# Kernel tuning notes

Measured on AMD Instinct MI355X. Metric: run time of the kernel, lower is better.

The kernel has to match this reference:

```python
import jax, jax.numpy as jnp
import numpy as np

B, NC, T = 256, 10, 4096
EPS, ALPHA, GAMMA, MU = 0.2, 0.5, 1e-4, 8e-4


def setup_inputs() -> dict:
    key = jax.random.key(0)
    k1, k2, k3 = jax.random.split(key, 3)
    scores = jax.random.uniform(k1, (B * NC, T), dtype=jnp.float32)
    attw = jax.random.uniform(k2, (B * NC, T), dtype=jnp.float32)
    # first half abnormal (label=1), second half normal (label=0), as pfu.unbag assumes
    label = jnp.concatenate([jnp.ones(B // 2, jnp.int32), jnp.zeros(B // 2, jnp.int32)])
    seqlen = jax.random.randint(k3, (B,), 128, T + 1, dtype=jnp.int32)
    return {"scores": scores, "attw": attw, "label": label, "seqlen": seqlen}


def _bce_neg(p, mask, slen):  # BCE vs all-zeros target, mean over valid length
    l = jnp.maximum(jnp.log(1.0 - p), -100.0)  # torch BCELoss clamps log at -100
    return -jnp.sum(jnp.where(mask, l, 0.0), axis=1) / slen


def _bce_pos(p, mask, slen):  # BCE vs all-ones target
    l = jnp.maximum(jnp.log(p), -100.0)
    return -jnp.sum(jnp.where(mask, l, 0.0), axis=1) / slen


def reference(scores, attw, label, seqlen):
    Bn = label.shape[0]
    nc = scores.shape[0] // Bn
    Tn = scores.shape[1]
    # pfu.uncrop(x, 'mean'): average over crops -> [B, T]
    sc = scores.reshape(Bn, nc, Tn).mean(axis=1)
    aw = attw.reshape(Bn, nc, Tn).mean(axis=1)
    bdiv = Bn // 2
    # pfu.unbag: abnormal = first half (label==1), normal = second half
    S1, A1, sl1i = sc[:bdiv], aw[:bdiv], seqlen[:bdiv]
    S0, A0, sl0i = sc[bdiv:], aw[bdiv:], seqlen[bdiv:]
    sl1 = sl1i.astype(jnp.float32)
    sl0 = sl0i.astype(jnp.float32)
    t = jnp.arange(Tn)[None, :]
    m1 = t < sl1i[:, None]  # valid-position masks (ragged slicing)
    m0 = t < sl0i[:, None]
    SA0 = A0 * S0
    SA1 = A1 * S1

    def theta(A, m):  # (max - min) * eps + min over valid region
        mx = jnp.max(jnp.where(m, A, -jnp.inf), axis=1)
        mn = jnp.min(jnp.where(m, A, jnp.inf), axis=1)
        return (mx - mn) * EPS + mn

    sup0 = (A0 < theta(A0, m0)[:, None]) & m0
    sup1 = (A1 < theta(A1, m1)[:, None]) & m1
    SSO0 = S0 * sup0
    SSA0 = SA0 * sup0
    SSO1 = S1 * sup1
    SSA1 = SA1 * sup1

    LC_SO = _bce_neg(S0, m0, sl0) + _bce_pos(S1, m1, sl1)
    LC_SA = _bce_neg(SA0, m0, sl0) + _bce_pos(SA1, m1, sl1)
    LC_SSO = _bce_neg(SSO0, m0, sl0) + _bce_pos(SSO1, m1, sl1)
    LC_SSA = _bce_neg(SSA0, m0, sl0) + _bce_pos(SSA1, m1, sl1)

    LN_1 = jnp.sum(jnp.where(m1, jnp.abs(A1), 0.0), axis=1)

    # LG_0 / LG_1 are overwritten in the torch loop -> only last batch item counts
    LG_0 = jnp.sum(jnp.where(m0[-1], A0[-1] ** 2, 0.0)) / sl0[-1]
    # cur_stp = 1 < M  ->  lg1_tmp = SO_1 (soft guide)
    LG_1 = jnp.sum(jnp.where(m1[-1], (A1[-1] - S1[-1]) ** 2, 0.0)) / sl1[-1]

    dm0 = t[:, : Tn - 1] < (sl0i - 1)[:, None]  # valid adjacent-diff positions
    dm1 = t[:, : Tn - 1] < (sl1i - 1)[:, None]

    def smt(S, dm):
        return jnp.sum(jnp.where(dm, (S[:, :-1] - S[:, 1:]) ** 2, 0.0), axis=1)

    LSmt = smt(S0, dm0) + smt(S1, dm1) + smt(SA0, dm0) + smt(SA1, dm1)
    LSpr = (jnp.sum(jnp.where(m0, S0, 0.0), axis=1) + jnp.sum(jnp.where(m1, S1, 0.0), axis=1)
            + jnp.sum(jnp.where(m0, SA0, 0.0), axis=1) + jnp.sum(jnp.where(m1, SA1, 0.0), axis=1))

    return jnp.stack([
        (ALPHA * LC_SO).mean(),          # slclas_og
        (ALPHA * LC_SA).mean(),          # slclas_att
        ((1.0 - ALPHA) * LC_SSO).mean(), # slclas_supog
        ((1.0 - ALPHA) * LC_SSA).mean(), # slclas_supatt
        (GAMMA * LN_1).mean(),           # norm_1
        LG_0,                            # guide_0
        LG_1,                            # guide_1
        (MU * LSmt).mean(),              # smooth
        LSpr.mean(),                     # sparse
    ])
```

## Files before the change

kernel.cpp:

```cpp
#include <hip/hip_runtime.h>
#include <math.h>

constexpr int   T_DIM = 4096;
constexpr int   NC    = 10;
constexpr int   NTHR  = 1024;
constexpr int   NWAVE = NTHR / 64;
constexpr int   PSTRIDE = 16;

constexpr float EPS_C   = 0.2f;
constexpr float ALPHA_C = 0.5f;
constexpr float GAMMA_C = 1e-4f;
constexpr float MU_C    = 8e-4f;

__global__ __launch_bounds__(NTHR) void mbs_pass1(
    const float* __restrict__ scores,
    const float* __restrict__ attw,
    const int*   __restrict__ seqlen,
    float*       __restrict__ part,
    int B)
{
    __shared__ float s_lds[T_DIM];
    __shared__ float a_lds[T_DIM];
    __shared__ float red_mx[NWAVE];
    __shared__ float red_mn[NWAVE];
    __shared__ float red_sum[NWAVE][8];
    __shared__ float sh_theta;

    const int tid  = threadIdx.x;
    const int lane = tid & 63;
    const int wid  = tid >> 6;
    const int b    = blockIdx.x;
    const int slen = seqlen[b];
    const bool pos = b < (B >> 1);
    const int t0   = tid * 4;
    const bool active = t0 < slen;

    float4 s4 = make_float4(0.f, 0.f, 0.f, 0.f);
    float4 a4 = make_float4(0.f, 0.f, 0.f, 0.f);
    if (active) {
        const size_t rowbase = (size_t)b * NC * T_DIM + t0;
#pragma unroll
        for (int c = 0; c < NC; ++c) {
            const float4 sv = *reinterpret_cast<const float4*>(scores + rowbase + (size_t)c * T_DIM);
            const float4 av = *reinterpret_cast<const float4*>(attw   + rowbase + (size_t)c * T_DIM);
            s4.x += sv.x; s4.y += sv.y; s4.z += sv.z; s4.w += sv.w;
            a4.x += av.x; a4.y += av.y; a4.z += av.z; a4.w += av.w;
        }
        const float invNC = 1.0f / (float)NC;
        s4.x *= invNC; s4.y *= invNC; s4.z *= invNC; s4.w *= invNC;
        a4.x *= invNC; a4.y *= invNC; a4.z *= invNC; a4.w *= invNC;

        reinterpret_cast<float4*>(s_lds)[tid] = s4;
        reinterpret_cast<float4*>(a_lds)[tid] = a4;
    }

    const float sarr[4] = {s4.x, s4.y, s4.z, s4.w};
    const float aarr[4] = {a4.x, a4.y, a4.z, a4.w};

    float amax = -INFINITY, amin = INFINITY;
    if (active) {
#pragma unroll
        for (int j = 0; j < 4; ++j) {
            if (t0 + j < slen) {
                amax = fmaxf(amax, aarr[j]);
                amin = fminf(amin, aarr[j]);
            }
        }
    }
#pragma unroll
    for (int off = 32; off; off >>= 1) {
        amax = fmaxf(amax, __shfl_down(amax, off, 64));
        amin = fminf(amin, __shfl_down(amin, off, 64));
    }
    if (lane == 0) { red_mx[wid] = amax; red_mn[wid] = amin; }
    __syncthreads();
    if (tid == 0) {
        float mx = red_mx[0], mn = red_mn[0];
#pragma unroll
        for (int w = 1; w < NWAVE; ++w) {
            mx = fmaxf(mx, red_mx[w]);
            mn = fminf(mn, red_mn[w]);
        }
        sh_theta = (mx - mn) * EPS_C + mn;
    }
    __syncthreads();
    const float theta = sh_theta;

    float v0 = 0.f, v1 = 0.f, v2 = 0.f, v3 = 0.f,
          v4 = 0.f, v5 = 0.f, v6 = 0.f, v7 = 0.f;
    const bool isLG = (b == (B >> 1) - 1) || (b == B - 1);

    if (active) {
#pragma unroll
        for (int j = 0; j < 4; ++j) {
            const int t   = t0 + j;
            const float s  = sarr[j];
            const float a  = aarr[j];
            const float sa = s * a;
            if (t < slen) {
                const bool sup = a < theta;
                if (pos) {
                    const float ls  = fmaxf(__logf(s),  -100.0f);
                    const float lsa = fmaxf(__logf(sa), -100.0f);
                    v0 += ls;
                    v1 += lsa;
                    v2 += sup ? ls  : -100.0f;
                    v3 += sup ? lsa : -100.0f;
                    v4 += fabsf(a);
                    if (isLG) v5 += (a - s) * (a - s);
                } else {
                    const float ls  = fmaxf(__logf(1.0f - s),  -100.0f);
                    const float lsa = fmaxf(__logf(1.0f - sa), -100.0f);
                    v0 += ls;
                    v1 += lsa;
                    if (sup) { v2 += ls; v3 += lsa; }
                    if (isLG) v5 += a * a;
                }
                v7 += s + sa;
            }
            if (t < slen - 1) {
                const float s2 = (j < 3) ? sarr[j + 1] : s_lds[t + 1];
                const float a2 = (j < 3) ? aarr[j + 1] : a_lds[t + 1];
                const float ds  = s  - s2;
                const float dsa = sa - s2 * a2;
                v6 += ds * ds + dsa * dsa;
            }
        }
    }

    float vals[8] = {v0, v1, v2, v3, v4, v5, v6, v7};
#pragma unroll
    for (int k = 0; k < 8; ++k) {
#pragma unroll
        for (int off = 32; off; off >>= 1)
            vals[k] += __shfl_down(vals[k], off, 64);
    }
    if (lane == 0) {
#pragma unroll
        for (int k = 0; k < 8; ++k) red_sum[wid][k] = vals[k];
    }
    __syncthreads();

    if (tid == 0) {
        float tot[8];
#pragma unroll
        for (int k = 0; k < 8; ++k) tot[k] = 0.f;
        for (int w = 0; w < NWAVE; ++w)
#pragma unroll
            for (int k = 0; k < 8; ++k) tot[k] += red_sum[w][k];

        const float inv_slen = 1.0f / (float)slen;
        const float invB2    = 2.0f / (float)B;

        float* p = part + (size_t)b * PSTRIDE;
        p[0] = ALPHA_C          * (-tot[0] * inv_slen) * invB2;
        p[1] = ALPHA_C          * (-tot[1] * inv_slen) * invB2;
        p[2] = (1.0f - ALPHA_C) * (-tot[2] * inv_slen) * invB2;
        p[3] = (1.0f - ALPHA_C) * (-tot[3] * inv_slen) * invB2;
        p[4] = pos ? (GAMMA_C * tot[4] * invB2) : 0.0f;
        p[5] = (b == B - 1)        ? tot[5] * inv_slen : 0.0f;
        p[6] = (b == (B >> 1) - 1) ? tot[5] * inv_slen : 0.0f;
        p[7] = MU_C * tot[6] * invB2;
        p[8] = tot[7] * invB2;
    }
}

__global__ __launch_bounds__(64) void mbs_pass2(
    const float* __restrict__ part,
    float*       __restrict__ out,
    int B)
{
    float acc[9];
#pragma unroll
    for (int k = 0; k < 9; ++k) acc[k] = 0.f;
    for (int r = (int)threadIdx.x; r < B; r += 64) {
        const float* p = part + (size_t)r * PSTRIDE;
#pragma unroll
        for (int k = 0; k < 9; ++k) acc[k] += p[k];
    }
#pragma unroll
    for (int k = 0; k < 9; ++k) {
#pragma unroll
        for (int off = 32; off; off >>= 1)
            acc[k] += __shfl_down(acc[k], off, 64);
    }
    if (threadIdx.x == 0) {
#pragma unroll
        for (int k = 0; k < 9; ++k) out[k] = acc[k];
    }
}

extern "C" void kernel_launch(void* const* d_in, const int* in_sizes, int n_in,
                              void* d_out, int out_size, void* d_ws, size_t ws_size,
                              hipStream_t stream) {
    const float* scores = (const float*)d_in[0];
    const float* attw   = (const float*)d_in[1];
    const int*   seqlen = (const int*)d_in[3];
    const int B = in_sizes[2];

    float* part = (float*)d_ws;

    mbs_pass1<<<dim3(B), dim3(NTHR), 0, stream>>>(scores, attw, seqlen, part, B);
    mbs_pass2<<<dim3(1), dim3(64), 0, stream>>>(part, (float*)d_out, B);
}
```

Measured before the change: 19.55 us.

## Split each row across four chunk blocks with global staging and last-block reduction

Each row now runs as four 256-thread blocks instead of one 1024-thread block, which raises the number of blocks in flight. The first kernel writes the crop means to global workspace along with per-chunk max/min and partial sums. The second kernel computes theta from the chunk extrema, rereads the means to get the suppressed and smoothness terms, and has the last block (chosen by an atomic counter) do the final reduction. This drops the separate reduction launch, but it adds a global round trip for the means and puts the log work in two passes.

Measured after the change: 40.32 us. +106.2%, slower.

```diff
diff --git a/kernel.cpp b/kernel.cpp
--- a/kernel.cpp
+++ b/kernel.cpp
@@ -3,124 +3,200 @@
 
 constexpr int   T_DIM = 4096;
 constexpr int   NC    = 10;
-constexpr int   NTHR  = 1024;
+constexpr int   CHUNK = 1024;
+constexpr int   NCH   = T_DIM / CHUNK;
+constexpr int   NTHR  = CHUNK / 4;
 constexpr int   NWAVE = NTHR / 64;
-constexpr int   PSTRIDE = 16;
 
 constexpr float EPS_C   = 0.2f;
 constexpr float ALPHA_C = 0.5f;
 constexpr float GAMMA_C = 1e-4f;
 constexpr float MU_C    = 8e-4f;
 
-__global__ __launch_bounds__(NTHR) void mbs_pass1(
+
+__global__ __launch_bounds__(NTHR) void mbs_k1(
     const float* __restrict__ scores,
     const float* __restrict__ attw,
     const int*   __restrict__ seqlen,
-    float*       __restrict__ part,
+    float*       __restrict__ ws,
     int B)
 {
-    __shared__ float s_lds[T_DIM];
-    __shared__ float a_lds[T_DIM];
-    __shared__ float red_mx[NWAVE];
-    __shared__ float red_mn[NWAVE];
-    __shared__ float red_sum[NWAVE][8];
-    __shared__ float sh_theta;
-
+    float* Smean = ws;
+    float* Amean = ws + (size_t)B * T_DIM;
+    float* cmax  = Amean + (size_t)B * T_DIM;
+    float* cmin  = cmax + (size_t)B * NCH;
+    float* P1    = cmin + (size_t)B * NCH;
+    unsigned int* cnt =
+        (unsigned int*)(P1 + (size_t)B * NCH * 8 + (size_t)B * NCH * 4);
+
+    const int bid  = blockIdx.x;
+    const int row  = bid / NCH;
+    const int ch   = bid - row * NCH;
     const int tid  = threadIdx.x;
     const int lane = tid & 63;
     const int wid  = tid >> 6;
-    const int b    = blockIdx.x;
-    const int slen = seqlen[b];
-    const bool pos = b < (B >> 1);
-    const int t0   = tid * 4;
+
+    if (bid == 0 && tid == 0) *cnt = 0u;
+
+    const int  slen   = seqlen[row];
+    const bool pos    = row < (B >> 1);
+    const bool isLG   = (row == (B >> 1) - 1) || (row == B - 1);
+    const int  t0     = ch * CHUNK + tid * 4;
     const bool active = t0 < slen;
 
     float4 s4 = make_float4(0.f, 0.f, 0.f, 0.f);
     float4 a4 = make_float4(0.f, 0.f, 0.f, 0.f);
     if (active) {
-        const size_t rowbase = (size_t)b * NC * T_DIM + t0;
+        const size_t base = (size_t)row * NC * T_DIM + t0;
 #pragma unroll
         for (int c = 0; c < NC; ++c) {
-            const float4 sv = *reinterpret_cast<const float4*>(scores + rowbase + (size_t)c * T_DIM);
-            const float4 av = *reinterpret_cast<const float4*>(attw   + rowbase + (size_t)c * T_DIM);
+            const float4 sv = *reinterpret_cast<const float4*>(scores + base + (size_t)c * T_DIM);
+            const float4 av = *reinterpret_cast<const float4*>(attw   + base + (size_t)c * T_DIM);
             s4.x += sv.x; s4.y += sv.y; s4.z += sv.z; s4.w += sv.w;
             a4.x += av.x; a4.y += av.y; a4.z += av.z; a4.w += av.w;
         }
         const float invNC = 1.0f / (float)NC;
         s4.x *= invNC; s4.y *= invNC; s4.z *= invNC; s4.w *= invNC;
         a4.x *= invNC; a4.y *= invNC; a4.z *= invNC; a4.w *= invNC;
-
-        reinterpret_cast<float4*>(s_lds)[tid] = s4;
-        reinterpret_cast<float4*>(a_lds)[tid] = a4;
+        *reinterpret_cast<float4*>(Smean + (size_t)row * T_DIM + t0) = s4;
+        *reinterpret_cast<float4*>(Amean + (size_t)row * T_DIM + t0) = a4;
     }
 
     const float sarr[4] = {s4.x, s4.y, s4.z, s4.w};
     const float aarr[4] = {a4.x, a4.y, a4.z, a4.w};
 
-    float amax = -INFINITY, amin = INFINITY;
+    float mx = -INFINITY, mn = INFINITY;
+    float v0 = 0.f, v1 = 0.f, v4 = 0.f, v5 = 0.f, v7 = 0.f;
     if (active) {
 #pragma unroll
         for (int j = 0; j < 4; ++j) {
-            if (t0 + j < slen) {
-                amax = fmaxf(amax, aarr[j]);
-                amin = fminf(amin, aarr[j]);
-            }
-        }
-    }
+            const int t = t0 + j;
+            if (t < slen) {
+                const float s  = sarr[j];
+                const float a  = aarr[j];
+                const float sa = s * a;
+                mx = fmaxf(mx, a);
+                mn = fminf(mn, a);
+                if (pos) {
+                    v0 += fmaxf(__logf(s),  -100.0f);
+                    v1 += fmaxf(__logf(sa), -100.0f);
+                    v4 += fabsf(a);
+                    if (isLG) v5 += (a - s) * (a - s);
+                } else {
+                    v0 += fmaxf(__logf(1.0f - s),  -100.0f);
+                    v1 += fmaxf(__logf(1.0f - sa), -100.0f);
+                    if (isLG) v5 += a * a;
+                }
+                v7 += s + sa;
+            }
+        }
+    }
+
+    float vals[7] = {mx, mn, v0, v1, v4, v5, v7};
 #pragma unroll
     for (int off = 32; off; off >>= 1) {
-        amax = fmaxf(amax, __shfl_down(amax, off, 64));
-        amin = fminf(amin, __shfl_down(amin, off, 64));
-    }
-    if (lane == 0) { red_mx[wid] = amax; red_mn[wid] = amin; }
+        vals[0] = fmaxf(vals[0], __shfl_down(vals[0], off, 64));
+        vals[1] = fminf(vals[1], __shfl_down(vals[1], off, 64));
+#pragma unroll
+        for (int k = 2; k < 7; ++k)
+            vals[k] += __shfl_down(vals[k], off, 64);
+    }
+    __shared__ float red[NWAVE][7];
+    if (lane == 0)
+#pragma unroll
+        for (int k = 0; k < 7; ++k) red[wid][k] = vals[k];
     __syncthreads();
+
     if (tid == 0) {
-        float mx = red_mx[0], mn = red_mn[0];
+        float tmx = red[0][0], tmn = red[0][1];
+        float t2 = red[0][2], t3 = red[0][3], t4 = red[0][4],
+              t5 = red[0][5], t6 = red[0][6];
 #pragma unroll
         for (int w = 1; w < NWAVE; ++w) {
-            mx = fmaxf(mx, red_mx[w]);
-            mn = fminf(mn, red_mn[w]);
-        }
-        sh_theta = (mx - mn) * EPS_C + mn;
-    }
-    __syncthreads();
-    const float theta = sh_theta;
-
-    float v0 = 0.f, v1 = 0.f, v2 = 0.f, v3 = 0.f,
-          v4 = 0.f, v5 = 0.f, v6 = 0.f, v7 = 0.f;
-    const bool isLG = (b == (B >> 1) - 1) || (b == B - 1);
-
+            tmx = fmaxf(tmx, red[w][0]);
+            tmn = fminf(tmn, red[w][1]);
+            t2 += red[w][2]; t3 += red[w][3]; t4 += red[w][4];
+            t5 += red[w][5]; t6 += red[w][6];
+        }
+        cmax[(size_t)row * NCH + ch] = tmx;
+        cmin[(size_t)row * NCH + ch] = tmn;
+
+        const float inv_slen = 1.0f / (float)slen;
+        const float invB2    = 2.0f / (float)B;
+        float* p = P1 + (size_t)bid * 8;
+        p[0] = ALPHA_C * (-t2 * inv_slen) * invB2;
+        p[1] = ALPHA_C * (-t3 * inv_slen) * invB2;
+        p[2] = pos ? (GAMMA_C * t4 * invB2) : 0.0f;
+        p[3] = (row == B - 1)        ? t5 * inv_slen : 0.0f;
+        p[4] = (row == (B >> 1) - 1) ? t5 * inv_slen : 0.0f;
+        p[5] = t6 * invB2;
+    }
+}
+
+__global__ __launch_bounds__(NTHR) void mbs_k2(
+    const int* __restrict__ seqlen,
+    float*     __restrict__ ws,
+    float*     __restrict__ out,
+    int B)
+{
+    float* Smean = ws;
+    float* Amean = ws + (size_t)B * T_DIM;
+    float* cmax  = Amean + (size_t)B * T_DIM;
+    float* cmin  = cmax + (size_t)B * NCH;
+    float* P1    = cmin + (size_t)B * NCH;
+    float* P2    = P1 + (size_t)B * NCH * 8;
+    unsigned int* cnt = (unsigned int*)(P2 + (size_t)B * NCH * 4);
+
+    const int bid  = blockIdx.x;
+    const int grid = gridDim.x;
+    const int row  = bid / NCH;
+    const int ch   = bid - row * NCH;
+    const int tid  = threadIdx.x;
+    const int lane = tid & 63;
+    const int wid  = tid >> 6;
+
+    const int  slen   = seqlen[row];
+    const bool pos    = row < (B >> 1);
+    const int  t0     = ch * CHUNK + tid * 4;
+    const bool active = t0 < slen;
+
+    float mx = -INFINITY, mn = INFINITY;
+#pragma unroll
+    for (int c = 0; c < NCH; ++c) {
+        mx = fmaxf(mx, cmax[(size_t)row * NCH + c]);
+        mn = fminf(mn, cmin[(size_t)row * NCH + c]);
+    }
+    const float theta = (mx - mn) * EPS_C + mn;
+
+    float v2 = 0.f, v3 = 0.f, v6 = 0.f;
     if (active) {
+        const float4 s4 = *reinterpret_cast<const float4*>(Smean + (size_t)row * T_DIM + t0);
+        const float4 a4 = *reinterpret_cast<const float4*>(Amean + (size_t)row * T_DIM + t0);
+        const float sarr[4] = {s4.x, s4.y, s4.z, s4.w};
+        const float aarr[4] = {a4.x, a4.y, a4.z, a4.w};
 #pragma unroll
         for (int j = 0; j < 4; ++j) {
-            const int t   = t0 + j;
+            const int t = t0 + j;
             const float s  = sarr[j];
             const float a  = aarr[j];
             const float sa = s * a;
             if (t < slen) {
                 const bool sup = a < theta;
                 if (pos) {
-                    const float ls  = fmaxf(__logf(s),  -100.0f);
-                    const float lsa = fmaxf(__logf(sa), -100.0f);
-                    v0 += ls;
-                    v1 += lsa;
-                    v2 += sup ? ls  : -100.0f;
-                    v3 += sup ? lsa : -100.0f;
-                    v4 += fabsf(a);
-                    if (isLG) v5 += (a - s) * (a - s);
-                } else {
-                    const float ls  = fmaxf(__logf(1.0f - s),  -100.0f);
-                    const float lsa = fmaxf(__logf(1.0f - sa), -100.0f);
-                    v0 += ls;
-                    v1 += lsa;
-                    if (sup) { v2 += ls; v3 += lsa; }
-                    if (isLG) v5 += a * a;
+                    v2 += sup ? fmaxf(__logf(s),  -100.0f) : -100.0f;
+                    v3 += sup ? fmaxf(__logf(sa), -100.0f) : -100.0f;
+                } else if (sup) {
+                    v2 += fmaxf(__logf(1.0f - s),  -100.0f);
+                    v3 += fmaxf(__logf(1.0f - sa), -100.0f);
                 }
-                v7 += s + sa;
             }
             if (t < slen - 1) {
-                const float s2 = (j < 3) ? sarr[j + 1] : s_lds[t + 1];
-                const float a2 = (j < 3) ? aarr[j + 1] : a_lds[t + 1];
+                float s2, a2;
+                if (j < 3) { s2 = sarr[j + 1]; a2 = aarr[j + 1]; }
+                else {
+                    s2 = Smean[(size_t)row * T_DIM + t + 1];
+                    a2 = Amean[(size_t)row * T_DIM + t + 1];
+                }
                 const float ds  = s  - s2;
                 const float dsa = sa - s2 * a2;
                 v6 += ds * ds + dsa * dsa;
@@ -128,65 +204,71 @@
         }
     }
 
-    float vals[8] = {v0, v1, v2, v3, v4, v5, v6, v7};
-#pragma unroll
-    for (int k = 0; k < 8; ++k) {
-#pragma unroll
-        for (int off = 32; off; off >>= 1)
+    float vals[3] = {v2, v3, v6};
+#pragma unroll
+    for (int off = 32; off; off >>= 1)
+#pragma unroll
+        for (int k = 0; k < 3; ++k)
             vals[k] += __shfl_down(vals[k], off, 64);
-    }
-    if (lane == 0) {
-#pragma unroll
-        for (int k = 0; k < 8; ++k) red_sum[wid][k] = vals[k];
-    }
+
+    __shared__ float red[NWAVE][3];
+    __shared__ int   sdone;
+    if (lane == 0)
+#pragma unroll
+        for (int k = 0; k < 3; ++k) red[wid][k] = vals[k];
     __syncthreads();
 
     if (tid == 0) {
-        float tot[8];
-#pragma unroll
-        for (int k = 0; k < 8; ++k) tot[k] = 0.f;
-        for (int w = 0; w < NWAVE; ++w)
-#pragma unroll
-            for (int k = 0; k < 8; ++k) tot[k] += red_sum[w][k];
-
+        float t2 = red[0][0], t3 = red[0][1], t6 = red[0][2];
+#pragma unroll
+        for (int w = 1; w < NWAVE; ++w) {
+            t2 += red[w][0]; t3 += red[w][1]; t6 += red[w][2];
+        }
         const float inv_slen = 1.0f / (float)slen;
         const float invB2    = 2.0f / (float)B;
-
-        float* p = part + (size_t)b * PSTRIDE;
-        p[0] = ALPHA_C          * (-tot[0] * inv_slen) * invB2;
-        p[1] = ALPHA_C          * (-tot[1] * inv_slen) * invB2;
-        p[2] = (1.0f - ALPHA_C) * (-tot[2] * inv_slen) * invB2;
-        p[3] = (1.0f - ALPHA_C) * (-tot[3] * inv_slen) * invB2;
-        p[4] = pos ? (GAMMA_C * tot[4] * invB2) : 0.0f;
-        p[5] = (b == B - 1)        ? tot[5] * inv_slen : 0.0f;
-        p[6] = (b == (B >> 1) - 1) ? tot[5] * inv_slen : 0.0f;
-        p[7] = MU_C * tot[6] * invB2;
-        p[8] = tot[7] * invB2;
-    }
-}
-
-__global__ __launch_bounds__(64) void mbs_pass2(
-    const float* __restrict__ part,
-    float*       __restrict__ out,
-    int B)
-{
-    float acc[9];
-#pragma unroll
-    for (int k = 0; k < 9; ++k) acc[k] = 0.f;
-    for (int r = (int)threadIdx.x; r < B; r += 64) {
-        const float* p = part + (size_t)r * PSTRIDE;
-#pragma unroll
-        for (int k = 0; k < 9; ++k) acc[k] += p[k];
-    }
-#pragma unroll
-    for (int k = 0; k < 9; ++k) {
+        float* p = P2 + (size_t)bid * 4;
+        p[0] = (1.0f - ALPHA_C) * (-t2 * inv_slen) * invB2;
+        p[1] = (1.0f - ALPHA_C) * (-t3 * inv_slen) * invB2;
+        p[2] = MU_C * t6 * invB2;
+        __threadfence();
+        const unsigned int old = atomicAdd(cnt, 1u);
+        sdone = (old == (unsigned int)(grid - 1)) ? 1 : 0;
+    }
+    __syncthreads();
+
+    if (sdone) {
+        __threadfence();
+        float acc[9];
+#pragma unroll
+        for (int k = 0; k < 9; ++k) acc[k] = 0.f;
+        for (int i = tid; i < grid; i += NTHR) {
+            const float* p1 = P1 + (size_t)i * 8;
+            const float* p2 = P2 + (size_t)i * 4;
+            acc[0] += p1[0]; acc[1] += p1[1];
+            acc[2] += p2[0]; acc[3] += p2[1];
+            acc[4] += p1[2]; acc[5] += p1[3];
+            acc[6] += p1[4]; acc[7] += p2[2];
+            acc[8] += p1[5];
+        }
 #pragma unroll
         for (int off = 32; off; off >>= 1)
-            acc[k] += __shfl_down(acc[k], off, 64);
-    }
-    if (threadIdx.x == 0) {
-#pragma unroll
-        for (int k = 0; k < 9; ++k) out[k] = acc[k];
+#pragma unroll
+            for (int k = 0; k < 9; ++k)
+                acc[k] += __shfl_down(acc[k], off, 64);
+        __shared__ float redf[NWAVE][9];
+        if (lane == 0)
+#pragma unroll
+            for (int k = 0; k < 9; ++k) redf[wid][k] = acc[k];
+        __syncthreads();
+        if (tid == 0) {
+#pragma unroll
+            for (int k = 0; k < 9; ++k) {
+                float s = redf[0][k];
+#pragma unroll
+                for (int w = 1; w < NWAVE; ++w) s += redf[w][k];
+                out[k] = s;
+            }
+        }
     }
 }
 
@@ -197,9 +279,10 @@
     const float* attw   = (const float*)d_in[1];
     const int*   seqlen = (const int*)d_in[3];
     const int B = in_sizes[2];
-
-    float* part = (float*)d_ws;
-
-    mbs_pass1<<<dim3(B), dim3(NTHR), 0, stream>>>(scores, attw, seqlen, part, B);
-    mbs_pass2<<<dim3(1), dim3(64), 0, stream>>>(part, (float*)d_out, B);
+    const int grid = B * NCH;
+
+    mbs_k1<<<dim3(grid), dim3(NTHR), 0, stream>>>(scores, attw, seqlen,
+                                                  (float*)d_ws, B);
+    mbs_k2<<<dim3(grid), dim3(NTHR), 0, stream>>>(seqlen, (float*)d_ws,
+                                                  (float*)d_out, B);
 }
```

## Split crop-mean into windowed kernel with direct global-to-LDS loads

Applied to the files above, without the earlier changes.

The crop-averaging stage moves into a new kernel launched over B*8 blocks, each handling one 512-column window. Each block loads all crops into LDS with global_load_lds, writes the mean rows to workspace and records per-window attention max/min. A second kernel combines the window max/min into theta and computes the losses from the stored means. The goal is more parallelism and better memory-level parallelism for the bandwidth-heavy crop reads, paid for by an extra launch and a workspace round trip for the means.

Result: slower. 26.70 us (+36.5%).

```diff
diff --git a/kernel.cpp b/kernel.cpp
--- a/kernel.cpp
+++ b/kernel.cpp
@@ -3,8 +3,10 @@
 
 constexpr int   T_DIM = 4096;
 constexpr int   NC    = 10;
-constexpr int   NTHR  = 1024;
-constexpr int   NWAVE = NTHR / 64;
+constexpr int   WIN   = 512;
+constexpr int   NQ    = T_DIM / WIN;
+constexpr int   K2THR = 1024;
+constexpr int   K2WAVE = K2THR / 64;
 constexpr int   PSTRIDE = 16;
 
 constexpr float EPS_C   = 0.2f;
@@ -12,88 +14,153 @@
 constexpr float GAMMA_C = 1e-4f;
 constexpr float MU_C    = 8e-4f;
 
-__global__ __launch_bounds__(NTHR) void mbs_pass1(
+
+__device__ __forceinline__ void gl_lds16(const float* g, float* l) {
+    __builtin_amdgcn_global_load_lds(
+        (const __attribute__((address_space(1))) void*)g,
+        (__attribute__((address_space(3))) void*)l, 16, 0, 0);
+}
+
+__global__ __launch_bounds__(256) void mbs_k1(
     const float* __restrict__ scores,
     const float* __restrict__ attw,
     const int*   __restrict__ seqlen,
-    float*       __restrict__ part,
+    float*       __restrict__ ws,
     int B)
 {
+    float* Smean = ws;
+    float* Amean = ws + (size_t)B * T_DIM;
+    float* cmax  = Amean + (size_t)B * T_DIM;
+    float* cmin  = cmax + (size_t)B * NQ;
+
+    __shared__ float sl[NC][WIN];
+    __shared__ float al[NC][WIN];
+
+    const int bid  = blockIdx.x;
+    const int row  = bid >> 3;
+    const int win  = bid & 7;
+    const int tid  = threadIdx.x;
+    const int lane = tid & 63;
+    const int w    = tid >> 6;
+    const int slen = seqlen[row];
+    const int c0   = win * WIN;
+
+    if (c0 >= slen) {
+        if (tid == 0) {
+            cmax[row * NQ + win] = -INFINITY;
+            cmin[row * NQ + win] =  INFINITY;
+        }
+        return;
+    }
+
+    const size_t rowbase = (size_t)row * NC * T_DIM;
+    const bool   hi      = (c0 + 256) < slen;
+#pragma unroll
+    for (int i = 0; i < 10; ++i) {
+        const int piece = w * 10 + i;
+        const int half  = piece / 20;
+        const int rem   = piece % 20;
+        const int c     = rem >> 1;
+        const int part  = rem & 1;
+        if (part == 0 || hi) {
+            const float* g = (half ? attw : scores)
+                           + rowbase + (size_t)c * T_DIM + c0 + part * 256 + lane * 4;
+            float* l = (half ? &al[0][0] : &sl[0][0]) + c * WIN + part * 256;
+            gl_lds16(g, l);
+        }
+    }
+    __syncthreads();
+
+    const size_t rowm = (size_t)row * T_DIM;
+    const int  cc  = 2 * tid;
+    const int  col = c0 + cc;
+    const bool act = col < slen;
+    float amx = -INFINITY, amn = INFINITY;
+    if (act) {
+        float s0 = 0.f, s1 = 0.f, a0 = 0.f, a1 = 0.f;
+#pragma unroll
+        for (int c = 0; c < NC; ++c) {
+            const float2 sv = *reinterpret_cast<const float2*>(&sl[c][cc]);
+            const float2 av = *reinterpret_cast<const float2*>(&al[c][cc]);
+            s0 += sv.x; s1 += sv.y;
+            a0 += av.x; a1 += av.y;
+        }
+        const float2 sm = make_float2(s0 * 0.1f, s1 * 0.1f);
+        const float2 am = make_float2(a0 * 0.1f, a1 * 0.1f);
+        *reinterpret_cast<float2*>(Smean + rowm + col) = sm;
+        *reinterpret_cast<float2*>(Amean + rowm + col) = am;
+        amx = am.x; amn = am.x;
+        if (col + 1 < slen) { amx = fmaxf(amx, am.y); amn = fminf(amn, am.y); }
+    }
+
+#pragma unroll
+    for (int off = 32; off; off >>= 1) {
+        amx = fmaxf(amx, __shfl_down(amx, off, 64));
+        amn = fminf(amn, __shfl_down(amn, off, 64));
+    }
+    __syncthreads();
+    if (lane == 0) { sl[0][w] = amx; sl[0][4 + w] = amn; }
+    __syncthreads();
+    if (tid == 0) {
+        const float mx = fmaxf(fmaxf(sl[0][0], sl[0][1]), fmaxf(sl[0][2], sl[0][3]));
+        const float mn = fminf(fminf(sl[0][4], sl[0][5]), fminf(sl[0][6], sl[0][7]));
+        cmax[row * NQ + win] = mx;
+        cmin[row * NQ + win] = mn;
+    }
+}
+
+__global__ __launch_bounds__(K2THR) void mbs_k2(
+    const int*   __restrict__ seqlen,
+    const float* __restrict__ ws,
+    float*       __restrict__ part2,
+    int B)
+{
+    const float* Smean = ws;
+    const float* Amean = ws + (size_t)B * T_DIM;
+    const float* cmax  = Amean + (size_t)B * T_DIM;
+    const float* cmin  = cmax + (size_t)B * NQ;
+
     __shared__ float s_lds[T_DIM];
     __shared__ float a_lds[T_DIM];
-    __shared__ float red_mx[NWAVE];
-    __shared__ float red_mn[NWAVE];
-    __shared__ float red_sum[NWAVE][8];
-    __shared__ float sh_theta;
-
+    __shared__ float red_sum[K2WAVE][8];
+
+    const int b    = blockIdx.x;
     const int tid  = threadIdx.x;
     const int lane = tid & 63;
     const int wid  = tid >> 6;
-    const int b    = blockIdx.x;
     const int slen = seqlen[b];
     const bool pos = b < (B >> 1);
+    const bool isLG = (b == (B >> 1) - 1) || (b == B - 1);
     const int t0   = tid * 4;
     const bool active = t0 < slen;
+
+    float mx = -INFINITY, mn = INFINITY;
+#pragma unroll
+    for (int c = 0; c < NQ; ++c) {
+        mx = fmaxf(mx, cmax[b * NQ + c]);
+        mn = fminf(mn, cmin[b * NQ + c]);
+    }
+    const float theta = (mx - mn) * EPS_C + mn;
 
     float4 s4 = make_float4(0.f, 0.f, 0.f, 0.f);
     float4 a4 = make_float4(0.f, 0.f, 0.f, 0.f);
     if (active) {
-        const size_t rowbase = (size_t)b * NC * T_DIM + t0;
-#pragma unroll
-        for (int c = 0; c < NC; ++c) {
-            const float4 sv = *reinterpret_cast<const float4*>(scores + rowbase + (size_t)c * T_DIM);
-            const float4 av = *reinterpret_cast<const float4*>(attw   + rowbase + (size_t)c * T_DIM);
-            s4.x += sv.x; s4.y += sv.y; s4.z += sv.z; s4.w += sv.w;
-            a4.x += av.x; a4.y += av.y; a4.z += av.z; a4.w += av.w;
-        }
-        const float invNC = 1.0f / (float)NC;
-        s4.x *= invNC; s4.y *= invNC; s4.z *= invNC; s4.w *= invNC;
-        a4.x *= invNC; a4.y *= invNC; a4.z *= invNC; a4.w *= invNC;
-
+        s4 = *reinterpret_cast<const float4*>(Smean + (size_t)b * T_DIM + t0);
+        a4 = *reinterpret_cast<const float4*>(Amean + (size_t)b * T_DIM + t0);
         reinterpret_cast<float4*>(s_lds)[tid] = s4;
         reinterpret_cast<float4*>(a_lds)[tid] = a4;
     }
+    __syncthreads();
 
     const float sarr[4] = {s4.x, s4.y, s4.z, s4.w};
     const float aarr[4] = {a4.x, a4.y, a4.z, a4.w};
 
-    float amax = -INFINITY, amin = INFINITY;
-    if (active) {
-#pragma unroll
-        for (int j = 0; j < 4; ++j) {
-            if (t0 + j < slen) {
-                amax = fmaxf(amax, aarr[j]);
-                amin = fminf(amin, aarr[j]);
-            }
-        }
-    }
-#pragma unroll
-    for (int off = 32; off; off >>= 1) {
-        amax = fmaxf(amax, __shfl_down(amax, off, 64));
-        amin = fminf(amin, __shfl_down(amin, off, 64));
-    }
-    if (lane == 0) { red_mx[wid] = amax; red_mn[wid] = amin; }
-    __syncthreads();
-    if (tid == 0) {
-        float mx = red_mx[0], mn = red_mn[0];
-#pragma unroll
-        for (int w = 1; w < NWAVE; ++w) {
-            mx = fmaxf(mx, red_mx[w]);
-            mn = fminf(mn, red_mn[w]);
-        }
-        sh_theta = (mx - mn) * EPS_C + mn;
-    }
-    __syncthreads();
-    const float theta = sh_theta;
-
     float v0 = 0.f, v1 = 0.f, v2 = 0.f, v3 = 0.f,
           v4 = 0.f, v5 = 0.f, v6 = 0.f, v7 = 0.f;
-    const bool isLG = (b == (B >> 1) - 1) || (b == B - 1);
-
     if (active) {
 #pragma unroll
         for (int j = 0; j < 4; ++j) {
-            const int t   = t0 + j;
+            const int t = t0 + j;
             const float s  = sarr[j];
             const float a  = aarr[j];
             const float sa = s * a;
@@ -130,29 +197,26 @@
 
     float vals[8] = {v0, v1, v2, v3, v4, v5, v6, v7};
 #pragma unroll
-    for (int k = 0; k < 8; ++k) {
+    for (int k = 0; k < 8; ++k)
 #pragma unroll
         for (int off = 32; off; off >>= 1)
             vals[k] += __shfl_down(vals[k], off, 64);
-    }
-    if (lane == 0) {
+    if (lane == 0)
 #pragma unroll
         for (int k = 0; k < 8; ++k) red_sum[wid][k] = vals[k];
-    }
     __syncthreads();
 
     if (tid == 0) {
         float tot[8];
 #pragma unroll
         for (int k = 0; k < 8; ++k) tot[k] = 0.f;
-        for (int w = 0; w < NWAVE; ++w)
-#pragma unroll
-            for (int k = 0; k < 8; ++k) tot[k] += red_sum[w][k];
+        for (int w2 = 0; w2 < K2WAVE; ++w2)
+#pragma unroll
+            for (int k = 0; k < 8; ++k) tot[k] += red_sum[w2][k];
 
         const float inv_slen = 1.0f / (float)slen;
         const float invB2    = 2.0f / (float)B;
-
-        float* p = part + (size_t)b * PSTRIDE;
+        float* p = part2 + (size_t)b * PSTRIDE;
         p[0] = ALPHA_C          * (-tot[0] * inv_slen) * invB2;
         p[1] = ALPHA_C          * (-tot[1] * inv_slen) * invB2;
         p[2] = (1.0f - ALPHA_C) * (-tot[2] * inv_slen) * invB2;
@@ -165,8 +229,8 @@
     }
 }
 
-__global__ __launch_bounds__(64) void mbs_pass2(
-    const float* __restrict__ part,
+__global__ __launch_bounds__(64) void mbs_k3(
+    const float* __restrict__ part2,
     float*       __restrict__ out,
     int B)
 {
@@ -174,20 +238,18 @@
 #pragma unroll
     for (int k = 0; k < 9; ++k) acc[k] = 0.f;
     for (int r = (int)threadIdx.x; r < B; r += 64) {
-        const float* p = part + (size_t)r * PSTRIDE;
+        const float* p = part2 + (size_t)r * PSTRIDE;
 #pragma unroll
         for (int k = 0; k < 9; ++k) acc[k] += p[k];
     }
 #pragma unroll
-    for (int k = 0; k < 9; ++k) {
+    for (int k = 0; k < 9; ++k)
 #pragma unroll
         for (int off = 32; off; off >>= 1)
             acc[k] += __shfl_down(acc[k], off, 64);
-    }
-    if (threadIdx.x == 0) {
+    if (threadIdx.x == 0)
 #pragma unroll
         for (int k = 0; k < 9; ++k) out[k] = acc[k];
-    }
 }
 
 extern "C" void kernel_launch(void* const* d_in, const int* in_sizes, int n_in,
@@ -198,8 +260,10 @@
     const int*   seqlen = (const int*)d_in[3];
     const int B = in_sizes[2];
 
-    float* part = (float*)d_ws;
-
-    mbs_pass1<<<dim3(B), dim3(NTHR), 0, stream>>>(scores, attw, seqlen, part, B);
-    mbs_pass2<<<dim3(1), dim3(64), 0, stream>>>(part, (float*)d_out, B);
-}
+    float* ws    = (float*)d_ws;
+    float* part2 = ws + (size_t)B * T_DIM * 2 + (size_t)B * NQ * 2;
+
+    mbs_k1<<<dim3(B * NQ), dim3(256), 0, stream>>>(scores, attw, seqlen, ws, B);
+    mbs_k2<<<dim3(B), dim3(K2THR), 0, stream>>>(seqlen, ws, part2, B);
+    mbs_k3<<<dim3(1), dim3(64), 0, stream>>>(part2, (float*)d_out, B);
+}
```
